# Optimization experiments

Hardware: AMD Instinct MI355X
Metric: run time of the kernel (lower is better)

Reference implementation:

```python
import jax, jax.numpy as jnp
import numpy as np

NH = 16   # n_heads
HD = 64   # head_size
EMB = 1024  # n_embd = NH * HD
B, T = 4, 2048


def setup_inputs() -> dict:
    key = jax.random.key(0)
    k1, k2, k3 = jax.random.split(key, 3)
    x = jax.random.normal(k1, (B, T, EMB), dtype=jnp.float32)
    # torch Linear(in, out, bias=False): weight [out,in]; we store transposed [in,out]
    W_attn = jax.random.normal(k2, (EMB, 3 * NH * HD), dtype=jnp.float32) * (EMB ** -0.5)
    W_proj = jax.random.normal(k3, (NH * HD, EMB), dtype=jnp.float32) * ((NH * HD) ** -0.5)
    b_proj = jnp.zeros((EMB,), dtype=jnp.float32)
    return {"x": x, "W_attn": W_attn, "W_proj": W_proj, "b_proj": b_proj}


def reference(x, W_attn, W_proj, b_proj):
    Bq, Tq, C = x.shape
    qkv = x @ W_attn                      # [B,T,3*Nh*H]
    qs, ks, vs = jnp.split(qkv, 3, axis=2)
    def to_heads(t):                      # [B,T,Nh*H] -> [B,Nh,T,H]
        return t.reshape(Bq, Tq, NH, HD).transpose(0, 2, 1, 3)
    q, k, v = to_heads(qs), to_heads(ks), to_heads(vs)
    scores = jnp.einsum('bnth,bnsh->bnts', q, k) * (HD ** -0.5)  # [B,Nh,T,T]
    causal = jnp.tril(jnp.ones((Tq, Tq), dtype=bool))
    scores = jnp.where(causal, scores, -jnp.inf)
    attn = jax.nn.softmax(scores, axis=-1)
    # dropout is identity in eval mode
    y = jnp.einsum('bnts,bnsh->bnth', attn, v)                   # [B,Nh,T,H]
    y = y.transpose(0, 2, 1, 3).reshape(Bq, Tq, NH * HD)
    return y @ W_proj + b_proj
```

## Files before the change

kernel.cpp:

```cpp
#include <hip/hip_runtime.h>
#include <hip/hip_bf16.h>

#define NH 16
#define HD 64
#define EMB 1024
#define BB 4
#define TT 2048
#define MTOT (BB*TT)
#define N1 (3*NH*HD)
#define KD EMB

#define QSCALE 0.18033688011112042f
#define FMAX 14.0f

typedef __bf16 bf16x8 __attribute__((ext_vector_type(8)));
typedef __bf16 bf16x4 __attribute__((ext_vector_type(4)));
typedef float  f32x4  __attribute__((ext_vector_type(4)));
typedef __hip_bfloat16 hbf;

__device__ __forceinline__ void async_copy16(const hbf* g, hbf* l) {
    __builtin_amdgcn_global_load_lds(
        (const __attribute__((address_space(1))) void*)g,
        (__attribute__((address_space(3))) void*)l, 16, 0, 0);
}

__device__ __forceinline__ bf16x4 pack4(float x0, float x1, float x2, float x3) {
    union { bf16x4 v; hbf a[4]; } u;
    u.a[0] = __float2bfloat16(x0);
    u.a[1] = __float2bfloat16(x1);
    u.a[2] = __float2bfloat16(x2);
    u.a[3] = __float2bfloat16(x3);
    return u.v;
}


__global__ __launch_bounds__(256) void f32_to_bf16_v4(const float* __restrict__ in,
                                                      hbf* __restrict__ out, int n4) {
    int i = blockIdx.x * blockDim.x + threadIdx.x;
    if (i < n4) {
        float4 v = ((const float4*)in)[i];
        *(bf16x4*)(out + 4 * (size_t)i) = pack4(v.x, v.y, v.z, v.w);
    }
}

__global__ __launch_bounds__(256) void f32_to_bf16_T(const float* __restrict__ in,
                                                     hbf* __restrict__ out, int R, int C) {
    __shared__ float T[64][65];
    int bc = blockIdx.x % (C / 64), br = blockIdx.x / (C / 64);
    int r0 = br * 64, c0 = bc * 64;
    int tr = threadIdx.x >> 6, tc = threadIdx.x & 63;
    #pragma unroll
    for (int i = 0; i < 16; ++i)
        T[4 * i + tr][tc] = in[(size_t)(r0 + 4 * i + tr) * C + c0 + tc];
    __syncthreads();
    #pragma unroll
    for (int i = 0; i < 16; ++i)
        out[(size_t)(c0 + 4 * i + tr) * R + r0 + tc] = __float2bfloat16(T[tc][4 * i + tr]);
}


template<int NBN, int MODE>
__global__ __launch_bounds__(256, 4) void gemm_v2(
    const hbf* __restrict__ A, const hbf* __restrict__ Bt,
    hbf* __restrict__ qh, hbf* __restrict__ kh, hbf* __restrict__ vt,
    const float* __restrict__ bias, float* __restrict__ out)
{
    constexpr int NKT = KD / 32;
    __shared__ __align__(16) hbf As[2 * 128 * 32];
    __shared__ __align__(16) hbf Bs[2 * 128 * 32];

    int tid = threadIdx.x;
    int wv = tid >> 6, lane = tid & 63;
    int g = lane >> 4, c = lane & 15;
    int wm = wv >> 1, wn = wv & 1;
    int wg = (blockIdx.x & 7) * (8 * NBN) + (blockIdx.x >> 3);
    int bn = wg % NBN, bm = wg / NBN;
    int m0 = bm * 128, n0 = bn * 128;

    int sr = tid >> 2;
    int sgc = (tid & 3) ^ (sr & 3);
    const hbf* Asrc0 = A  + (size_t)(m0 + sr) * KD + sgc * 8;
    const hbf* Asrc1 = A  + (size_t)(m0 + 64 + sr) * KD + sgc * 8;
    const hbf* Bsrc0 = Bt + (size_t)(n0 + sr) * KD + sgc * 8;
    const hbf* Bsrc1 = Bt + (size_t)(n0 + 64 + sr) * KD + sgc * 8;
    int ld0 = (tid & ~63) * 8, ld1 = 2048 + (tid & ~63) * 8;

#define STG(tt, buf) { \
    async_copy16(Asrc0 + (tt) * 32, As + (buf) * 4096 + ld0); \
    async_copy16(Asrc1 + (tt) * 32, As + (buf) * 4096 + ld1); \
    async_copy16(Bsrc0 + (tt) * 32, Bs + (buf) * 4096 + ld0); \
    async_copy16(Bsrc1 + (tt) * 32, Bs + (buf) * 4096 + ld1); }

    int x3 = c & 3;
    int ao = (wm * 64 + c) * 32 + ((g ^ x3) << 3);
    int bo = (wn * 64 + c) * 32 + ((g ^ x3) << 3);

    f32x4 acc[4][4];
    #pragma unroll
    for (int i = 0; i < 4; ++i)
        #pragma unroll
        for (int j = 0; j < 4; ++j) acc[i][j] = (f32x4){0.f, 0.f, 0.f, 0.f};

    STG(0, 0);
    STG(1, 1);
    asm volatile("s_waitcnt vmcnt(4)" ::: "memory");
    asm volatile("s_barrier" ::: "memory");
    __builtin_amdgcn_sched_barrier(0);

    for (int t = 0; t < NKT; ++t) {
        int cur = t & 1;
        const hbf* Ab = As + cur * 4096;
        const hbf* Bb = Bs + cur * 4096;
        bf16x8 af[4], bfr[4];
        #pragma unroll
        for (int i = 0; i < 4; ++i) af[i] = *(const bf16x8*)(Ab + ao + i * 512);
        #pragma unroll
        for (int j = 0; j < 4; ++j) bfr[j] = *(const bf16x8*)(Bb + bo + j * 512);
        asm volatile("s_waitcnt lgkmcnt(0)" ::: "memory");
        __builtin_amdgcn_sched_barrier(0);
        asm volatile("s_barrier" ::: "memory");
        __builtin_amdgcn_sched_barrier(0);
        if (t + 2 < NKT) STG(t + 2, cur);
        __builtin_amdgcn_s_setprio(1);
        #pragma unroll
        for (int i = 0; i < 4; ++i)
            #pragma unroll
            for (int j = 0; j < 4; ++j)
                acc[i][j] = __builtin_amdgcn_mfma_f32_16x16x32_bf16(af[i], bfr[j], acc[i][j], 0, 0, 0);
        __builtin_amdgcn_s_setprio(0);
        if (t + 2 < NKT) { asm volatile("s_waitcnt vmcnt(4)" ::: "memory"); }
        else             { asm volatile("s_waitcnt vmcnt(0)" ::: "memory"); }
        asm volatile("s_barrier" ::: "memory");
        __builtin_amdgcn_sched_barrier(0);
    }
#undef STG

    if constexpr (MODE == 0) {
        int colbase = n0 + wn * 64;
        int which = colbase >> 10;
        int h = (colbase & 1023) >> 6;
        int b = m0 / TT;
        int trow = (m0 % TT) + wm * 64;
        if (which < 2) {
            float scale = (which == 0) ? QSCALE : 1.0f;
            hbf* dst = ((which == 0) ? qh : kh) + ((size_t)b * NH + h) * TT * HD;
            #pragma unroll
            for (int i = 0; i < 4; ++i)
                #pragma unroll
                for (int j = 0; j < 4; ++j) {
                    int d = j * 16 + c;
                    #pragma unroll
                    for (int r = 0; r < 4; ++r) {
                        int trw = trow + i * 16 + g * 4 + r;
                        dst[(size_t)trw * HD + d] = __float2bfloat16(acc[i][j][r] * scale);
                    }
                }
        } else {
            hbf* dst = vt + ((size_t)b * NH + h) * TT * HD;
            #pragma unroll
            for (int i = 0; i < 4; ++i)
                #pragma unroll
                for (int j = 0; j < 4; ++j) {
                    int d = j * 16 + c;
                    #pragma unroll
                    for (int r = 0; r < 4; ++r) {
                        int trw = trow + i * 16 + g * 4 + r;
                        dst[(size_t)d * TT + trw] = __float2bfloat16(acc[i][j][r]);
                    }
                }
        }
    } else {
        #pragma unroll
        for (int i = 0; i < 4; ++i)
            #pragma unroll
            for (int j = 0; j < 4; ++j) {
                int col = n0 + wn * 64 + j * 16 + c;
                float bv = bias[col];
                #pragma unroll
                for (int r = 0; r < 4; ++r) {
                    int row = m0 + wm * 64 + i * 16 + g * 4 + r;
                    out[(size_t)row * EMB + col] = acc[i][j][r] + bv;
                }
            }
    }
}


__global__ __launch_bounds__(512, 4) void attn(
    const hbf* __restrict__ qh, const hbf* __restrict__ kh, const hbf* __restrict__ vt,
    hbf* __restrict__ y)
{
    __shared__ __align__(16) hbf Ks[2 * 128 * 64];
    __shared__ __align__(16) hbf Vs[2 * 64 * 128];
    __shared__ __align__(16) hbf Ps[8][16 * 64];

    int tid = threadIdx.x;
    int wv = tid >> 6, lane = tid & 63;
    int g = lane >> 4, c = lane & 15;
    int c7 = c & 7;

    int bidx = blockIdx.x;
    int bh = (bidx & 7) | (((bidx >> 6) & 7) << 3);
    int pi = (bidx >> 3) & 7;
    int b = bh >> 4, h = bh & 15;

    const hbf* Q = qh + (size_t)bh * TT * HD;
    const hbf* K = kh + (size_t)bh * TT * HD;
    const hbf* V = vt + (size_t)bh * TT * HD;
    hbf* Pq = &Ps[wv][0];

#define ASTG(ss, buf) { \
    int k0s = (ss) * 128; \
    _Pragma("unroll") for (int it = 0; it < 2; ++it) { \
        int e = it * 4096 + tid * 8; \
        int key = e >> 6, sblk = (e >> 3) & 7; \
        int dblk = sblk ^ (key & 7); \
        async_copy16(K + (size_t)(k0s + key) * HD + dblk * 8, \
                     Ks + (buf) * 8192 + it * 4096 + (tid & ~63) * 8); } \
    _Pragma("unroll") for (int it = 0; it < 2; ++it) { \
        int e = it * 4096 + tid * 8; \
        int dim = e >> 7, kb = (e >> 3) & 15; \
        int skb = kb ^ (dim & 7); \
        async_copy16(V + (size_t)dim * TT + k0s + skb * 8, \
                     Vs + (buf) * 8192 + it * 4096 + (tid & ~63) * 8); } }

    union { bf16x8 v; hbf a[8]; } uo;
    #pragma unroll
    for (int i = 0; i < 8; ++i) uo.a[i] = __float2bfloat16(1.0f);
    const bf16x8 ones8 = uo.v;

    #pragma unroll
    for (int pass = 0; pass < 2; ++pass) {
        int sst = pass ? (15 - pi) : pi;
        int qb = sst * 128;
        int q0 = qb + wv * 16;
        int kend = q0 + 16;
        int S = sst + 1;

        bf16x8 aq0 = *(const bf16x8*)(Q + (size_t)(q0 + c) * HD + g * 8);
        bf16x8 aq1 = *(const bf16x8*)(Q + (size_t)(q0 + c) * HD + 32 + g * 8);

        f32x4 lacc = (f32x4){0.f, 0.f, 0.f, 0.f};
        f32x4 o[4];
        #pragma unroll
        for (int d = 0; d < 4; ++d) o[d] = (f32x4){0.f, 0.f, 0.f, 0.f};

        ASTG(0, 0);
        if (S > 1) {
            ASTG(1, 1);
            asm volatile("s_waitcnt vmcnt(4)" ::: "memory");
        } else {
            asm volatile("s_waitcnt vmcnt(0)" ::: "memory");
        }
        asm volatile("s_barrier" ::: "memory");
        __builtin_amdgcn_sched_barrier(0);

        for (int s = 0; s < S; ++s) {
            int k0 = s * 128;
            const hbf* Kb = Ks + (s & 1) * 8192;
            const hbf* Vb = Vs + (s & 1) * 8192;

            #pragma unroll
            for (int ch = 0; ch < 2; ++ch) {
                int c64 = k0 + ch * 64;
                if (c64 < kend) {
                    f32x4 sv[4];
                    #pragma unroll
                    for (int t = 0; t < 4; ++t) {
                        int kt = c64 + 16 * t;
                        if (kt < kend) {
                            int rb = (ch * 64 + 16 * t + c) * 64;
                            bf16x8 kf0 = *(const bf16x8*)(Kb + rb + ((g ^ c7) << 3));
                            bf16x8 kf1 = *(const bf16x8*)(Kb + rb + (((4 + g) ^ c7) << 3));
                            f32x4 a = (f32x4){-FMAX, -FMAX, -FMAX, -FMAX};
                            a = __builtin_amdgcn_mfma_f32_16x16x32_bf16(kf0, aq0, a, 0, 0, 0);
                            a = __builtin_amdgcn_mfma_f32_16x16x32_bf16(kf1, aq1, a, 0, 0, 0);
                            if (kt == q0) {
                                #pragma unroll
                                for (int r = 0; r < 4; ++r)
                                    a[r] = (g * 4 + r <= c) ? a[r] : -1e30f;
                            }
                            sv[t] = a;
                        } else
                            sv[t] = (f32x4){-1e30f, -1e30f, -1e30f, -1e30f};
                    }
                    #pragma unroll
                    for (int t = 0; t < 4; ++t) {
                        f32x4 e;
                        #pragma unroll
                        for (int r = 0; r < 4; ++r) e[r] = __builtin_amdgcn_exp2f(sv[t][r]);
                        *(bf16x4*)(Pq + c * 64 + (((2 * t + (g >> 1)) ^ c7) << 3) + ((g & 1) << 2)) =
                            pack4(e[0], e[1], e[2], e[3]);
                    }
                    #pragma unroll
                    for (int sc = 0; sc < 2; ++sc) {
                        if (c64 + 32 * sc < kend) {
                            bf16x8 pf = *(const bf16x8*)(Pq + c * 64 + (((4 * sc + g) ^ c7) << 3));
                            lacc = __builtin_amdgcn_mfma_f32_16x16x32_bf16(ones8, pf, lacc, 0, 0, 0);
                            #pragma unroll
                            for (int d = 0; d < 4; ++d) {
                                int dim = d * 16 + c;
                                bf16x8 vf = *(const bf16x8*)(Vb + dim * 128 +
                                              (((ch * 8 + 4 * sc + g) ^ c7) << 3));
                                o[d] = __builtin_amdgcn_mfma_f32_16x16x32_bf16(vf, pf, o[d], 0, 0, 0);
                            }
                        }
                    }
                }
            }

            asm volatile("s_barrier" ::: "memory");
            __builtin_amdgcn_sched_barrier(0);
            if (s + 2 < S) {
                ASTG(s + 2, s & 1);
                asm volatile("s_waitcnt vmcnt(4)" ::: "memory");
            } else if (s + 1 < S) {
                asm volatile("s_waitcnt vmcnt(0)" ::: "memory");
            }
            asm volatile("s_barrier" ::: "memory");
            __builtin_amdgcn_sched_barrier(0);
        }

        float inv = 1.0f / lacc[0];
        #pragma unroll
        for (int d = 0; d < 4; ++d) {
            *(bf16x4*)(y + (size_t)(b * TT + q0 + c) * EMB + h * HD + d * 16 + g * 4) =
                pack4(o[d][0] * inv, o[d][1] * inv, o[d][2] * inv, o[d][3] * inv);
        }
    }
#undef ASTG
}


extern "C" void kernel_launch(void* const* d_in, const int* in_sizes, int n_in,
                              void* d_out, int out_size, void* d_ws, size_t ws_size,
                              hipStream_t stream)
{
    const float* x      = (const float*)d_in[0];
    const float* W_attn = (const float*)d_in[1];
    const float* W_proj = (const float*)d_in[2];
    const float* b_proj = (const float*)d_in[3];
    float* out = (float*)d_out;

    char* ws = (char*)d_ws;
    hbf* xb    = (hbf*)ws; ws += (size_t)MTOT * KD * 2;
    hbf* wab_t = (hbf*)ws; ws += (size_t)N1 * KD * 2;
    hbf* wpb_t = (hbf*)ws; ws += (size_t)EMB * EMB * 2;
    hbf* qh    = (hbf*)ws; ws += (size_t)MTOT * EMB * 2;
    hbf* kh    = (hbf*)ws; ws += (size_t)MTOT * EMB * 2;
    hbf* vt    = (hbf*)ws; ws += (size_t)MTOT * EMB * 2;
    hbf* yb    = (hbf*)ws; ws += (size_t)MTOT * EMB * 2;

    f32_to_bf16_v4<<<(MTOT * KD / 4 + 255) / 256, 256, 0, stream>>>(x, xb, MTOT * KD / 4);
    f32_to_bf16_T<<<(KD / 64) * (N1 / 64), 256, 0, stream>>>(W_attn, wab_t, KD, N1);
    f32_to_bf16_T<<<(KD / 64) * (EMB / 64), 256, 0, stream>>>(W_proj, wpb_t, KD, EMB);

    gemm_v2<N1 / 128, 0><<<(MTOT / 128) * (N1 / 128), 256, 0, stream>>>(
        xb, wab_t, qh, kh, vt, nullptr, nullptr);
    attn<<<BB * NH * 8, 512, 0, stream>>>(qh, kh, vt, yb);
    gemm_v2<EMB / 128, 1><<<(MTOT / 128) * (EMB / 128), 256, 0, stream>>>(
        yb, wpb_t, nullptr, nullptr, nullptr, b_proj, out);
}
```

Measured before the change: 250.9 us.

## Rework GEMM into 128x256 tiles with 512 threads and split staged pipeline

Replaces the 128x128, 256-thread GEMM with a 128x256 tile computed by 8 waves, using a K-step of 64 instead of 32. The LDS staging is split into A, B-low and B-high chunks that are interleaved with half-tile MFMA phases, so loads for the next step overlap with compute. The aim is more operand reuse per LDS byte, fewer K iterations and fewer barriers per unit of work. In exchange it uses more shared memory and more barriers per step, and it halves the block count, which could hurt occupancy or tail balance.

```diff
diff --git a/kernel.cpp b/kernel.cpp
--- a/kernel.cpp
+++ b/kernel.cpp
@@ -59,81 +59,106 @@
 }
 
 
+#define GBAR  asm volatile("s_barrier" ::: "memory")
+#define GLGKM { asm volatile("s_waitcnt lgkmcnt(0)" ::: "memory"); __builtin_amdgcn_sched_barrier(0); }
+#define GVM2  asm volatile("s_waitcnt vmcnt(2)" ::: "memory")
+
 template<int NBN, int MODE>
-__global__ __launch_bounds__(256, 4) void gemm_v2(
+__global__ __launch_bounds__(512, 2) void gemm_v3(
     const hbf* __restrict__ A, const hbf* __restrict__ Bt,
     hbf* __restrict__ qh, hbf* __restrict__ kh, hbf* __restrict__ vt,
     const float* __restrict__ bias, float* __restrict__ out)
 {
-    constexpr int NKT = KD / 32;
-    __shared__ __align__(16) hbf As[2 * 128 * 32];
-    __shared__ __align__(16) hbf Bs[2 * 128 * 32];
+    constexpr int NKT = KD / 64;
+    constexpr int NIT = NKT / 2;
+    constexpr int GRID = (MTOT / 128) * NBN;
+    __shared__ __align__(16) hbf As[2 * 128 * 64];
+    __shared__ __align__(16) hbf Bs[2 * 256 * 64];
 
     int tid = threadIdx.x;
     int wv = tid >> 6, lane = tid & 63;
     int g = lane >> 4, c = lane & 15;
-    int wm = wv >> 1, wn = wv & 1;
-    int wg = (blockIdx.x & 7) * (8 * NBN) + (blockIdx.x >> 3);
+    int wm = wv >> 2, wn = wv & 3;
+    int xr = c & 7;
+    int wg = (blockIdx.x & 7) * (GRID / 8) + (blockIdx.x >> 3);
     int bn = wg % NBN, bm = wg / NBN;
-    int m0 = bm * 128, n0 = bn * 128;
-
-    int sr = tid >> 2;
-    int sgc = (tid & 3) ^ (sr & 3);
-    const hbf* Asrc0 = A  + (size_t)(m0 + sr) * KD + sgc * 8;
-    const hbf* Asrc1 = A  + (size_t)(m0 + 64 + sr) * KD + sgc * 8;
-    const hbf* Bsrc0 = Bt + (size_t)(n0 + sr) * KD + sgc * 8;
-    const hbf* Bsrc1 = Bt + (size_t)(n0 + 64 + sr) * KD + sgc * 8;
-    int ld0 = (tid & ~63) * 8, ld1 = 2048 + (tid & ~63) * 8;
-
-#define STG(tt, buf) { \
-    async_copy16(Asrc0 + (tt) * 32, As + (buf) * 4096 + ld0); \
-    async_copy16(Asrc1 + (tt) * 32, As + (buf) * 4096 + ld1); \
-    async_copy16(Bsrc0 + (tt) * 32, Bs + (buf) * 4096 + ld0); \
-    async_copy16(Bsrc1 + (tt) * 32, Bs + (buf) * 4096 + ld1); }
-
-    int x3 = c & 3;
-    int ao = (wm * 64 + c) * 32 + ((g ^ x3) << 3);
-    int bo = (wn * 64 + c) * 32 + ((g ^ x3) << 3);
-
+    int m0 = bm * 128, n0 = bn * 256;
+
+    int srow = tid >> 3;
+    int sgc = (tid & 7) ^ (srow & 7);
+    const hbf* pA = A  + (size_t)(m0 + srow) * KD + sgc * 8;
+    const hbf* pB = Bt + (size_t)(n0 + srow) * KD + sgc * 8;
+    int ldsd = (tid & ~63) * 8;
+
+#define STG_A(t, buf)  { async_copy16(pA + (t)*64,                  As + (buf)*8192  + ldsd); \
+                         async_copy16(pA + (size_t)64*KD  + (t)*64, As + (buf)*8192  + 4096 + ldsd); }
+#define STG_B01(t, buf){ async_copy16(pB + (t)*64,                  Bs + (buf)*16384 + ldsd); \
+                         async_copy16(pB + (size_t)64*KD  + (t)*64, Bs + (buf)*16384 + 4096 + ldsd); }
+#define STG_B23(t, buf){ async_copy16(pB + (size_t)128*KD + (t)*64, Bs + (buf)*16384 + 8192 + ldsd); \
+                         async_copy16(pB + (size_t)192*KD + (t)*64, Bs + (buf)*16384 + 12288 + ldsd); }
+
+    int arow = wm * 64 + c;
+    int brow = wn * 64 + c;
+    bf16x8 af[4][2], bfr[2][2];
     f32x4 acc[4][4];
     #pragma unroll
     for (int i = 0; i < 4; ++i)
         #pragma unroll
         for (int j = 0; j < 4; ++j) acc[i][j] = (f32x4){0.f, 0.f, 0.f, 0.f};
 
-    STG(0, 0);
-    STG(1, 1);
-    asm volatile("s_waitcnt vmcnt(4)" ::: "memory");
-    asm volatile("s_barrier" ::: "memory");
+#define LDA(buf) { _Pragma("unroll") for (int mi = 0; mi < 4; ++mi) { \
+    const hbf* ap = As + (buf)*8192 + (arow + mi*16) * 64; \
+    af[mi][0] = *(const bf16x8*)(ap + ((g ^ xr) << 3)); \
+    af[mi][1] = *(const bf16x8*)(ap + (((4 + g) ^ xr) << 3)); } }
+#define LDB(buf, nq) { _Pragma("unroll") for (int k2 = 0; k2 < 2; ++k2) { \
+    const hbf* bp = Bs + (buf)*16384 + (brow + (nq)*32 + k2*16) * 64; \
+    bfr[k2][0] = *(const bf16x8*)(bp + ((g ^ xr) << 3)); \
+    bfr[k2][1] = *(const bf16x8*)(bp + (((4 + g) ^ xr) << 3)); } }
+#define MM(nq) { __builtin_amdgcn_s_setprio(1); \
+    _Pragma("unroll") for (int mi = 0; mi < 4; ++mi) \
+      _Pragma("unroll") for (int k2 = 0; k2 < 2; ++k2) { \
+        acc[mi][(nq)*2+k2] = __builtin_amdgcn_mfma_f32_16x16x32_bf16(af[mi][0], bfr[k2][0], acc[mi][(nq)*2+k2], 0, 0, 0); \
+        acc[mi][(nq)*2+k2] = __builtin_amdgcn_mfma_f32_16x16x32_bf16(af[mi][1], bfr[k2][1], acc[mi][(nq)*2+k2], 0, 0, 0); } \
+    __builtin_amdgcn_s_setprio(0); }
+
+    STG_A(0, 0); STG_B01(0, 0); STG_B23(0, 0);
+    STG_A(1, 1);
+    GVM2;
+    GBAR;
     __builtin_amdgcn_sched_barrier(0);
 
-    for (int t = 0; t < NKT; ++t) {
-        int cur = t & 1;
-        const hbf* Ab = As + cur * 4096;
-        const hbf* Bb = Bs + cur * 4096;
-        bf16x8 af[4], bfr[4];
-        #pragma unroll
-        for (int i = 0; i < 4; ++i) af[i] = *(const bf16x8*)(Ab + ao + i * 512);
-        #pragma unroll
-        for (int j = 0; j < 4; ++j) bfr[j] = *(const bf16x8*)(Bb + bo + j * 512);
-        asm volatile("s_waitcnt lgkmcnt(0)" ::: "memory");
+    for (int i = 0; i < NIT - 1; ++i) {
+        int t = 2 * i;
+        LDA(0); LDB(0, 0); STG_B01(t + 1, 1);
+        GBAR; GLGKM; MM(0); GBAR;
+        LDB(0, 1); STG_B23(t + 1, 1); STG_A(t + 2, 0);
+        GBAR; GLGKM; MM(1);
+        GVM2; GBAR;
+        LDA(1); LDB(1, 0); STG_B01(t + 2, 0);
+        GBAR; GLGKM; MM(0); GBAR;
+        LDB(1, 1); STG_B23(t + 2, 0); STG_A(t + 3, 1);
+        GBAR; GLGKM; MM(1);
+        GVM2; GBAR;
         __builtin_amdgcn_sched_barrier(0);
-        asm volatile("s_barrier" ::: "memory");
-        __builtin_amdgcn_sched_barrier(0);
-        if (t + 2 < NKT) STG(t + 2, cur);
-        __builtin_amdgcn_s_setprio(1);
-        #pragma unroll
-        for (int i = 0; i < 4; ++i)
-            #pragma unroll
-            for (int j = 0; j < 4; ++j)
-                acc[i][j] = __builtin_amdgcn_mfma_f32_16x16x32_bf16(af[i], bfr[j], acc[i][j], 0, 0, 0);
-        __builtin_amdgcn_s_setprio(0);
-        if (t + 2 < NKT) { asm volatile("s_waitcnt vmcnt(4)" ::: "memory"); }
-        else             { asm volatile("s_waitcnt vmcnt(0)" ::: "memory"); }
-        asm volatile("s_barrier" ::: "memory");
-        __builtin_amdgcn_sched_barrier(0);
-    }
-#undef STG
+    }
+    {
+        LDA(0); LDB(0, 0); STG_B01(NKT - 1, 1);
+        GBAR; GLGKM; MM(0); GBAR;
+        LDB(0, 1); STG_B23(NKT - 1, 1);
+        GBAR; GLGKM; MM(1);
+        asm volatile("s_waitcnt vmcnt(0)" ::: "memory");
+        GBAR;
+        LDA(1); LDB(1, 0);
+        GBAR; GLGKM; MM(0); GBAR;
+        LDB(1, 1);
+        GBAR; GLGKM; MM(1);
+    }
+#undef STG_A
+#undef STG_B01
+#undef STG_B23
+#undef LDA
+#undef LDB
+#undef MM
 
     if constexpr (MODE == 0) {
         int colbase = n0 + wn * 64;
@@ -145,41 +170,41 @@
             float scale = (which == 0) ? QSCALE : 1.0f;
             hbf* dst = ((which == 0) ? qh : kh) + ((size_t)b * NH + h) * TT * HD;
             #pragma unroll
-            for (int i = 0; i < 4; ++i)
+            for (int mi = 0; mi < 4; ++mi)
                 #pragma unroll
-                for (int j = 0; j < 4; ++j) {
-                    int d = j * 16 + c;
+                for (int nj = 0; nj < 4; ++nj) {
+                    int d = nj * 16 + c;
                     #pragma unroll
                     for (int r = 0; r < 4; ++r) {
-                        int trw = trow + i * 16 + g * 4 + r;
-                        dst[(size_t)trw * HD + d] = __float2bfloat16(acc[i][j][r] * scale);
+                        int trw = trow + mi * 16 + g * 4 + r;
+                        dst[(size_t)trw * HD + d] = __float2bfloat16(acc[mi][nj][r] * scale);
                     }
                 }
         } else {
             hbf* dst = vt + ((size_t)b * NH + h) * TT * HD;
             #pragma unroll
-            for (int i = 0; i < 4; ++i)
+            for (int mi = 0; mi < 4; ++mi)
                 #pragma unroll
-                for (int j = 0; j < 4; ++j) {
-                    int d = j * 16 + c;
+                for (int nj = 0; nj < 4; ++nj) {
+                    int d = nj * 16 + c;
                     #pragma unroll
                     for (int r = 0; r < 4; ++r) {
-                        int trw = trow + i * 16 + g * 4 + r;
-                        dst[(size_t)d * TT + trw] = __float2bfloat16(acc[i][j][r]);
+                        int trw = trow + mi * 16 + g * 4 + r;
+                        dst[(size_t)d * TT + trw] = __float2bfloat16(acc[mi][nj][r]);
                     }
                 }
         }
     } else {
         #pragma unroll
-        for (int i = 0; i < 4; ++i)
+        for (int mi = 0; mi < 4; ++mi)
             #pragma unroll
-            for (int j = 0; j < 4; ++j) {
-                int col = n0 + wn * 64 + j * 16 + c;
+            for (int nj = 0; nj < 4; ++nj) {
+                int col = n0 + wn * 64 + nj * 16 + c;
                 float bv = bias[col];
                 #pragma unroll
                 for (int r = 0; r < 4; ++r) {
-                    int row = m0 + wm * 64 + i * 16 + g * 4 + r;
-                    out[(size_t)row * EMB + col] = acc[i][j][r] + bv;
+                    int row = m0 + wm * 64 + mi * 16 + g * 4 + r;
+                    out[(size_t)row * EMB + col] = acc[mi][nj][r] + bv;
                 }
             }
     }
@@ -355,9 +380,9 @@
     f32_to_bf16_T<<<(KD / 64) * (N1 / 64), 256, 0, stream>>>(W_attn, wab_t, KD, N1);
     f32_to_bf16_T<<<(KD / 64) * (EMB / 64), 256, 0, stream>>>(W_proj, wpb_t, KD, EMB);
 
-    gemm_v2<N1 / 128, 0><<<(MTOT / 128) * (N1 / 128), 256, 0, stream>>>(
+    gemm_v3<N1 / 256, 0><<<(MTOT / 128) * (N1 / 256), 512, 0, stream>>>(
         xb, wab_t, qh, kh, vt, nullptr, nullptr);
     attn<<<BB * NH * 8, 512, 0, stream>>>(qh, kh, vt, yb);
-    gemm_v2<EMB / 128, 1><<<(MTOT / 128) * (EMB / 128), 256, 0, stream>>>(
+    gemm_v3<EMB / 256, 1><<<(MTOT / 128) * (EMB / 256), 512, 0, stream>>>(
         yb, wpb_t, nullptr, nullptr, nullptr, b_proj, out);
 }
```

Measured after the change: 260.7 us. 3.9% more time.
